# Performance work log

Measured on AMD Instinct MI355X. Metric: run time of the kernel, lower is better.

## Reference

```python
import jax, jax.numpy as jnp
import numpy as np

B, T, P, F = 32, 12, 128, 128          # batch, timesteps, n_patches, nhid
NODES_PER_PATCH = 64
HORIZON = 12
N_NODES = P * NODES_PER_PATCH          # 8192


def setup_inputs() -> dict:
    key = jax.random.key(0)
    k1, k2, k3, k4 = jax.random.split(key, 4)
    x = jax.random.normal(k1, (B, T, P, F), dtype=jnp.float32)
    # per-patch Linear weights/biases, stacked: W[p] maps (nhid*T) -> (nodes_p*horizon)
    W = jax.random.normal(k2, (P, T * F, NODES_PER_PATCH * HORIZON), dtype=jnp.float32) * 0.02
    b = jax.random.normal(k3, (P, NODES_PER_PATCH * HORIZON), dtype=jnp.float32) * 0.02
    # patch -> global node indices; a permutation (each node in exactly one patch)
    patch_node_map = jax.random.permutation(k4, jnp.arange(N_NODES, dtype=jnp.int64)).reshape(P, NODES_PER_PATCH)
    return {"x": x, "W": W, "b": b, "patch_node_map": patch_node_map}


def reference(x, W, b, patch_node_map):
    # rearrange 'b t p f -> b p (t f)'
    xr = jnp.transpose(x, (0, 2, 1, 3)).reshape(x.shape[0], P, T * F)
    # grouped GEMM: one Linear per patch
    out = jnp.einsum('bpi,pio->bpo', xr, W) + b          # [B, P, nodes*H]
    out = out.reshape(x.shape[0], P * NODES_PER_PATCH, HORIZON)
    # scatter patch-local node predictions to global node positions
    out_all = jnp.zeros((x.shape[0], N_NODES, HORIZON), dtype=x.dtype)
    out_all = out_all.at[:, patch_node_map.reshape(-1), :].set(out)
    return out_all
```

## Files before the change

kernel.cpp:

```cpp
#include <hip/hip_runtime.h>
#include <hip/hip_bf16.h>


constexpr int T      = 12;
constexpr int P      = 128;
constexpr int F      = 128;
constexpr int K      = T * F;
constexpr int N      = 768;
constexpr int NPP    = 64;
constexpr int H      = 12;
constexpr int NNODES = P * NPP;
constexpr int BN     = 128;
constexpr int NT     = N / BN;
constexpr int NSTEP  = K / 64;
constexpr int TPF    = T * P * F;
constexpr int PF     = P * F;

typedef __attribute__((ext_vector_type(8))) short        bf16x8;
typedef __attribute__((ext_vector_type(4))) float        f32x4;
typedef __attribute__((ext_vector_type(4))) unsigned int u32x4;

__device__ inline unsigned short f2bfu(float f) {
    return __bfloat16_as_ushort(__float2bfloat16(f));
}
__device__ inline unsigned int pk2(float lo, float hi) {
    return (unsigned int)f2bfu(lo) | ((unsigned int)f2bfu(hi) << 16);
}

__global__ __launch_bounds__(256, 3)
void patch_readout_kernel(const float* __restrict__ x,
                          const float* __restrict__ W,
                          const float* __restrict__ bias,
                          const int*   __restrict__ map,
                          float*       __restrict__ out)
{
    __shared__ short Wl[2][128 * 64];
    __shared__ short Xl[2][32 * 64];
    char* wl = (char*)&Wl[0][0];
    char* xl = (char*)&Xl[0][0];

    const int bid = blockIdx.y * NT + blockIdx.x;
    const int lgc = (bid & 7) * 96 + (bid >> 3);
    const int p   = lgc / NT;
    const int n0  = (lgc % NT) * BN;

    const int tid  = threadIdx.x;
    const int lane = tid & 63;
    const int wv   = tid >> 6;
    const int r    = lane & 15;
    const int c    = lane >> 4;

    const int koct = tid >> 5;
    const int q    = tid & 31;
    const float* wg = W + (size_t)p * K * N + (size_t)(8 * koct) * N + (n0 + 4 * q);

    const int xrow = tid >> 3;
    const int xsub = tid & 7;
    const float* xg  = x + (size_t)xrow * TPF + p * F + xsub * 8;
    const int    xwb = xrow * 128 + ((xsub * 16) ^ ((xrow & 7) << 4));

    f32x4 acc[2][2] = {};
    f32x4 ws[8];
    f32x4 xs[2];

    auto issue = [&](int kt) {
        const size_t kofs = (size_t)kt * 64 * N;
        #pragma unroll
        for (int j = 0; j < 8; ++j)
            ws[j] = *(const f32x4*)(wg + kofs + (size_t)j * N);
        const int xo = (kt >> 1) * PF + (kt & 1) * 64;
        xs[0] = *(const f32x4*)(xg + xo);
        xs[1] = *(const f32x4*)(xg + xo + 4);
    };

    auto writeLds = [&](int d) {
        #pragma unroll
        for (int i = 0; i < 4; ++i) {
            u32x4 wd;
            wd.x = pk2(ws[0][i], ws[1][i]);
            wd.y = pk2(ws[2][i], ws[3][i]);
            wd.z = pk2(ws[4][i], ws[5][i]);
            wd.w = pk2(ws[6][i], ws[7][i]);
            const int col = 4 * q + i;
            *(u32x4*)(wl + d * 16384 + col * 128 + ((koct * 16) ^ ((col & 7) << 4))) = wd;
        }
        bf16x8 xv;
        #pragma unroll
        for (int e = 0; e < 4; ++e) {
            xv[e]     = (short)f2bfu(xs[0][e]);
            xv[4 + e] = (short)f2bfu(xs[1][e]);
        }
        *(bf16x8*)(xl + d * 4096 + xwb) = xv;
    };

    auto compute = [&](int d) {
        #pragma unroll
        for (int kc = 0; kc < 2; ++kc) {
            bf16x8 af[2], bfr[2];
            #pragma unroll
            for (int mi = 0; mi < 2; ++mi) {
                const int row = mi * 16 + r;
                af[mi] = *(const bf16x8*)(xl + d * 4096 + row * 128 +
                                          ((kc * 64 + c * 16) ^ ((row & 7) << 4)));
            }
            #pragma unroll
            for (int ni = 0; ni < 2; ++ni) {
                const int col = wv * 32 + ni * 16 + r;
                bfr[ni] = *(const bf16x8*)(wl + d * 16384 + col * 128 +
                                           ((kc * 64 + c * 16) ^ ((col & 7) << 4)));
            }
            #pragma unroll
            for (int mi = 0; mi < 2; ++mi)
                #pragma unroll
                for (int ni = 0; ni < 2; ++ni)
                    acc[mi][ni] = __builtin_amdgcn_mfma_f32_16x16x32_bf16(
                        af[mi], bfr[ni], acc[mi][ni], 0, 0, 0);
        }
    };

    issue(0);
    writeLds(0);
    __syncthreads();
    issue(1);

    for (int kt = 0; kt < NSTEP; ++kt) {
        const int d = kt & 1;
        compute(d);
        if (kt < NSTEP - 1) {
            writeLds(d ^ 1);
            __syncthreads();
            if (kt < NSTEP - 2) issue(kt + 2);
        }
    }

    #pragma unroll
    for (int ni = 0; ni < 2; ++ni) {
        const int col = n0 + wv * 32 + ni * 16 + r;
        const int nl  = col / H;
        const int h   = col - nl * H;
        const int g   = map[p * NPP + nl];
        const float bv = bias[p * N + col];
        #pragma unroll
        for (int mi = 0; mi < 2; ++mi) {
            #pragma unroll
            for (int i = 0; i < 4; ++i) {
                const int b = mi * 16 + c * 4 + i;
                out[((size_t)b * NNODES + g) * H + h] = acc[mi][ni][i] + bv;
            }
        }
    }
}

extern "C" void kernel_launch(void* const* d_in, const int* in_sizes, int n_in,
                              void* d_out, int out_size, void* d_ws, size_t ws_size,
                              hipStream_t stream) {
    const float* x    = (const float*)d_in[0];
    const float* W    = (const float*)d_in[1];
    const float* bias = (const float*)d_in[2];
    const int*   map  = (const int*)d_in[3];
    float*       out  = (float*)d_out;

    dim3 grid(NT, P);
    dim3 block(256);
    patch_readout_kernel<<<grid, block, 0, stream>>>(x, W, bias, map, out);
}
```

Before: 135.2 us.

## Use 384-wide N tiles with whole-X LDS staging and 256-block grid

Each block now covers 384 output columns with 384 threads, so the grid shrinks to 256 blocks, one per (patch, half-N). The whole 32x1536 activation slice is converted to bf16 once and kept in LDS, and only W is streamed through a double buffer in 32-row K steps, with each wave computing a 32x64 tile. This is meant to cut redundant X loads and per-step X conversion and to raise MFMA work per barrier. The cost is a large LDS footprint (about 96KB for X plus 48KB for W) and one block per CU, which limits latency hiding and leaves 256 blocks for the 256 CUs.

After: 125.2 us. 1.08x faster.

```diff
diff --git a/kernel.cpp b/kernel.cpp
--- a/kernel.cpp
+++ b/kernel.cpp
@@ -10,9 +10,8 @@
 constexpr int NPP    = 64;
 constexpr int H      = 12;
 constexpr int NNODES = P * NPP;
-constexpr int BN     = 128;
-constexpr int NT     = N / BN;
-constexpr int NSTEP  = K / 64;
+constexpr int BN     = 384;
+constexpr int NSTEP  = 48;
 constexpr int TPF    = T * P * F;
 constexpr int PF     = P * F;
 
@@ -27,22 +26,22 @@
     return (unsigned int)f2bfu(lo) | ((unsigned int)f2bfu(hi) << 16);
 }
 
-__global__ __launch_bounds__(256, 3)
+__global__ __launch_bounds__(384, 1)
 void patch_readout_kernel(const float* __restrict__ x,
                           const float* __restrict__ W,
                           const float* __restrict__ bias,
                           const int*   __restrict__ map,
                           float*       __restrict__ out)
 {
-    __shared__ short Wl[2][128 * 64];
-    __shared__ short Xl[2][32 * 64];
-    char* wl = (char*)&Wl[0][0];
-    char* xl = (char*)&Xl[0][0];
+    __shared__ short Xs[32 * K];
+    __shared__ short Ws2[2][4 * BN * 8];
+    char* xl  = (char*)&Xs[0];
+    char* wlb = (char*)&Ws2[0][0];
 
-    const int bid = blockIdx.y * NT + blockIdx.x;
-    const int lgc = (bid & 7) * 96 + (bid >> 3);
-    const int p   = lgc / NT;
-    const int n0  = (lgc % NT) * BN;
+    const int bid = blockIdx.x;
+    const int lgc = (bid & 7) * 32 + (bid >> 3);
+    const int p   = lgc >> 1;
+    const int n0  = (lgc & 1) * BN;
 
     const int tid  = threadIdx.x;
     const int lane = tid & 63;
@@ -50,30 +49,20 @@
     const int r    = lane & 15;
     const int c    = lane >> 4;
 
-    const int koct = tid >> 5;
-    const int q    = tid & 31;
-    const float* wg = W + (size_t)p * K * N + (size_t)(8 * koct) * N + (n0 + 4 * q);
+    const int c2 = tid / 96;
+    const int q  = tid - c2 * 96;
+    const float* wg = W + (size_t)p * K * N + (size_t)(8 * c2) * N + (n0 + 4 * q);
 
-    const int xrow = tid >> 3;
-    const int xsub = tid & 7;
-    const float* xg  = x + (size_t)xrow * TPF + p * F + xsub * 8;
-    const int    xwb = xrow * 128 + ((xsub * 16) ^ ((xrow & 7) << 4));
+    f32x4 ws[8];
 
-    f32x4 acc[2][2] = {};
-    f32x4 ws[8];
-    f32x4 xs[2];
-
-    auto issue = [&](int kt) {
-        const size_t kofs = (size_t)kt * 64 * N;
+    auto issueW = [&](int s) {
         #pragma unroll
         for (int j = 0; j < 8; ++j)
-            ws[j] = *(const f32x4*)(wg + kofs + (size_t)j * N);
-        const int xo = (kt >> 1) * PF + (kt & 1) * 64;
-        xs[0] = *(const f32x4*)(xg + xo);
-        xs[1] = *(const f32x4*)(xg + xo + 4);
+            ws[j] = *(const f32x4*)(wg + (size_t)(s * 32 + j) * N);
     };
 
-    auto writeLds = [&](int d) {
+    auto writeW = [&](int d) {
+        char* wl = wlb + d * 24576 + c2 * 6144;
         #pragma unroll
         for (int i = 0; i < 4; ++i) {
             u32x4 wd;
@@ -82,60 +71,65 @@
             wd.z = pk2(ws[4][i], ws[5][i]);
             wd.w = pk2(ws[6][i], ws[7][i]);
             const int col = 4 * q + i;
-            *(u32x4*)(wl + d * 16384 + col * 128 + ((koct * 16) ^ ((col & 7) << 4))) = wd;
-        }
-        bf16x8 xv;
-        #pragma unroll
-        for (int e = 0; e < 4; ++e) {
-            xv[e]     = (short)f2bfu(xs[0][e]);
-            xv[4 + e] = (short)f2bfu(xs[1][e]);
-        }
-        *(bf16x8*)(xl + d * 4096 + xwb) = xv;
-    };
-
-    auto compute = [&](int d) {
-        #pragma unroll
-        for (int kc = 0; kc < 2; ++kc) {
-            bf16x8 af[2], bfr[2];
-            #pragma unroll
-            for (int mi = 0; mi < 2; ++mi) {
-                const int row = mi * 16 + r;
-                af[mi] = *(const bf16x8*)(xl + d * 4096 + row * 128 +
-                                          ((kc * 64 + c * 16) ^ ((row & 7) << 4)));
-            }
-            #pragma unroll
-            for (int ni = 0; ni < 2; ++ni) {
-                const int col = wv * 32 + ni * 16 + r;
-                bfr[ni] = *(const bf16x8*)(wl + d * 16384 + col * 128 +
-                                           ((kc * 64 + c * 16) ^ ((col & 7) << 4)));
-            }
-            #pragma unroll
-            for (int mi = 0; mi < 2; ++mi)
-                #pragma unroll
-                for (int ni = 0; ni < 2; ++ni)
-                    acc[mi][ni] = __builtin_amdgcn_mfma_f32_16x16x32_bf16(
-                        af[mi], bfr[ni], acc[mi][ni], 0, 0, 0);
+            *(u32x4*)(wl + ((col * 16) ^ (((col >> 3) & 7) << 4))) = wd;
         }
     };
 
-    issue(0);
-    writeLds(0);
-    __syncthreads();
-    issue(1);
+    auto stageX = [&]() {
+        const int row = tid / 12;
+        const int sub = tid - row * 12;
+        const float* xg = x + (size_t)row * TPF + (size_t)sub * PF + (size_t)p * F;
+        char* xw = xl + row * 3072;
+        const int sw = (row & 7) << 4;
+        #pragma unroll
+        for (int ci = 0; ci < 16; ++ci) {
+            f32x4 v0 = *(const f32x4*)(xg + ci * 8);
+            f32x4 v1 = *(const f32x4*)(xg + ci * 8 + 4);
+            bf16x8 xv;
+            xv[0] = (short)f2bfu(v0.x); xv[1] = (short)f2bfu(v0.y);
+            xv[2] = (short)f2bfu(v0.z); xv[3] = (short)f2bfu(v0.w);
+            xv[4] = (short)f2bfu(v1.x); xv[5] = (short)f2bfu(v1.y);
+            xv[6] = (short)f2bfu(v1.z); xv[7] = (short)f2bfu(v1.w);
+            *(bf16x8*)(xw + ((sub * 256 + ci * 16) ^ sw)) = xv;
+        }
+    };
 
-    for (int kt = 0; kt < NSTEP; ++kt) {
-        const int d = kt & 1;
-        compute(d);
-        if (kt < NSTEP - 1) {
-            writeLds(d ^ 1);
-            __syncthreads();
-            if (kt < NSTEP - 2) issue(kt + 2);
+    f32x4 acc[2][4] = {};
+
+    auto compute = [&](int s, int d) {
+        const char* wl = wlb + d * 24576 + c * 6144;
+        bf16x8 af[2];
+        #pragma unroll
+        for (int mi = 0; mi < 2; ++mi) {
+            const int row = mi * 16 + r;
+            af[mi] = *(const bf16x8*)(xl + row * 3072 +
+                                      ((s * 64 + c * 16) ^ ((row & 7) << 4)));
         }
+        #pragma unroll
+        for (int ni = 0; ni < 4; ++ni) {
+            const int col = wv * 64 + ni * 16 + r;
+            bf16x8 bf = *(const bf16x8*)(wl + ((col * 16) ^ (((col >> 3) & 7) << 4)));
+            #pragma unroll
+            for (int mi = 0; mi < 2; ++mi)
+                acc[mi][ni] = __builtin_amdgcn_mfma_f32_16x16x32_bf16(
+                    af[mi], bf, acc[mi][ni], 0, 0, 0);
+        }
+    };
+
+    issueW(0);
+    stageX();
+    writeW(0);
+
+    for (int s = 0; s < NSTEP; ++s) {
+        __syncthreads();
+        if (s < NSTEP - 1) issueW(s + 1);
+        compute(s, s & 1);
+        if (s < NSTEP - 1) writeW((s + 1) & 1);
     }
 
     #pragma unroll
-    for (int ni = 0; ni < 2; ++ni) {
-        const int col = n0 + wv * 32 + ni * 16 + r;
+    for (int ni = 0; ni < 4; ++ni) {
+        const int col = n0 + wv * 64 + ni * 16 + r;
         const int nl  = col / H;
         const int h   = col - nl * H;
         const int g   = map[p * NPP + nl];
@@ -160,7 +154,7 @@
     const int*   map  = (const int*)d_in[3];
     float*       out  = (float*)d_out;
 
-    dim3 grid(NT, P);
-    dim3 block(256);
+    dim3 grid(256);
+    dim3 block(384);
     patch_readout_kernel<<<grid, block, 0, stream>>>(x, W, bias, map, out);
 }
```
